# Optimization experiments

Measured on AMD Instinct MI355X. Metric: run time of the kernel, lower is better.

Reference implementation:

```python
import jax, jax.numpy as jnp
import numpy as np

D_MODEL = 1024
NUM_HEADS = 16
HEAD_DIM = D_MODEL // NUM_HEADS
B, T = 2, 2048


def setup_inputs() -> dict:
    key = jax.random.key(0)
    kx, kq, kk, kv, ko = jax.random.split(key, 5)
    s = 1.0 / np.sqrt(D_MODEL)  # ~Linear init scale
    return {
        "x": jax.random.normal(kx, (B, T, D_MODEL), dtype=jnp.float32),
        "Wq": jax.random.normal(kq, (D_MODEL, D_MODEL), dtype=jnp.float32) * s,
        "Wk": jax.random.normal(kk, (D_MODEL, D_MODEL), dtype=jnp.float32) * s,
        "Wv": jax.random.normal(kv, (D_MODEL, D_MODEL), dtype=jnp.float32) * s,
        "Wo": jax.random.normal(ko, (D_MODEL, D_MODEL), dtype=jnp.float32) * s,
    }


def reference(x, Wq, Wk, Wv, Wo):
    Bc, Tc, _ = x.shape
    H, D = NUM_HEADS, HEAD_DIM
    scale = jnp.sqrt(jnp.asarray(D, x.dtype))
    # torch Linear (bias=False): y = x @ W^T
    q = (x @ Wq.T).reshape(Bc, Tc, H, D).transpose(0, 2, 1, 3)  # [B,H,T,D]
    k = (x @ Wk.T).reshape(Bc, Tc, H, D).transpose(0, 2, 1, 3)
    v = (x @ Wv.T).reshape(Bc, Tc, H, D).transpose(0, 2, 1, 3)
    scores = jnp.einsum("bhtd,bhsd->bhts", q, k) / scale  # [B,H,T,T]
    # causal bias: upper triangle (strictly future positions) gets -1e9
    causal_bias = jnp.triu(jnp.ones((Tc, Tc), dtype=jnp.float32), k=1) * -1e9
    scores = scores + causal_bias
    weights = jax.nn.softmax(scores, axis=-1)
    # dropout is identity in eval / p=0
    out = jnp.einsum("bhts,bhsd->bhtd", weights, v)  # [B,H,T,D]
    out = out.transpose(0, 2, 1, 3).reshape(Bc, Tc, H * D)
    return out @ Wo.T
```

## Files before the change

### kernel.cpp

```cpp
#include <hip/hip_runtime.h>
#include <hip/hip_bf16.h>

typedef __bf16 bf16_t;
typedef __bf16 bf16x2 __attribute__((ext_vector_type(2)));
typedef __bf16 bf16x4 __attribute__((ext_vector_type(4)));
typedef __bf16 bf16x8 __attribute__((ext_vector_type(8)));
typedef float  f32x4  __attribute__((ext_vector_type(4)));
typedef int    i32x2  __attribute__((ext_vector_type(2)));

#define D_MODEL 1024
#define HEADS   16
#define HD      64
#define BB      2
#define TT      2048
#define MROWS   (BB*TT)

#define GLDS16(g, l) __builtin_amdgcn_global_load_lds( \
    (const __attribute__((address_space(1))) void*)(g), \
    (__attribute__((address_space(3))) void*)(l), 16, 0, 0)

static __device__ __forceinline__ int pack_bf16(float a, float b) {
    bf16x2 t; t[0] = (bf16_t)a; t[1] = (bf16_t)b;
    return __builtin_bit_cast(int, t);
}

__global__ __launch_bounds__(256) void cvt_all_kernel(const float* __restrict__ x,
                                                      const float* __restrict__ wq,
                                                      const float* __restrict__ wk,
                                                      const float* __restrict__ wv,
                                                      const float* __restrict__ wo,
                                                      bf16_t* __restrict__ dst) {
    const int i = blockIdx.x * 256 + threadIdx.x;
    const float* src;
    int s;
    if (i < 1048576) { src = x; s = i; }
    else {
        int j = i - 1048576;
        int w = j >> 18;
        s = j & 262143;
        src = (w == 0) ? wq : (w == 1) ? wk : (w == 2) ? wv : wo;
    }
    float4 v = reinterpret_cast<const float4*>(src)[s];
    bf16x4 o;
    o[0] = (bf16_t)v.x; o[1] = (bf16_t)v.y; o[2] = (bf16_t)v.z; o[3] = (bf16_t)v.w;
    reinterpret_cast<bf16x4*>(dst)[i] = o;
}

template<int MODE, int BN>
__global__ __launch_bounds__(256) void gemm_bt(const bf16_t* __restrict__ A,
                                               const bf16_t* __restrict__ Bw,
                                               void* __restrict__ Cout,
                                               int M, int N, int K) {
    constexpr int NI = BN / 32;
    __shared__ __align__(16) bf16_t As[128*32];
    __shared__ __align__(16) bf16_t Bs[BN*32];
    const int tid   = threadIdx.x;
    const int lane  = tid & 63;
    const int wave  = tid >> 6;
    const int col16 = lane & 15;
    const int quad  = lane >> 4;
    const int wrow  = (wave & 1) * 64;
    const int wcol  = (wave >> 1) * (BN / 2);
    const int bm    = blockIdx.y * 128;
    const int bn    = blockIdx.x * BN;

    const int lr = tid >> 2;
    const int lc = (tid & 3) * 8;

    const bf16_t* agp = &A [(size_t)(bm + lr)*K + lc];
    const bf16_t* bgp = &Bw[(size_t)(bn + lr)*K + lc];
    const size_t half = (size_t)64 * K;
    bf16_t* as_lo = &As[wave*512];
    bf16_t* as_hi = &As[2048 + wave*512];
    bf16_t* bs_lo = &Bs[wave*512];
    bf16_t* bs_hi = &Bs[2048 + wave*512];

    f32x4 acc[4][NI];
#pragma unroll
    for (int i = 0; i < 4; i++)
#pragma unroll
        for (int j = 0; j < NI; j++) acc[i][j] = (f32x4){0.f, 0.f, 0.f, 0.f};

    for (int k0 = 0; k0 < K; k0 += 32) {
        GLDS16(agp + k0,        as_lo);
        GLDS16(agp + half + k0, as_hi);
        GLDS16(bgp + k0,        bs_lo);
        if (BN == 128) GLDS16(bgp + half + k0, bs_hi);
        __syncthreads();

        bf16x8 af[4], bfr[NI];
#pragma unroll
        for (int mi = 0; mi < 4; mi++)
            af[mi] = *reinterpret_cast<const bf16x8*>(&As[(wrow + mi*16 + col16)*32 + quad*8]);
#pragma unroll
        for (int ni = 0; ni < NI; ni++)
            bfr[ni] = *reinterpret_cast<const bf16x8*>(&Bs[(wcol + ni*16 + col16)*32 + quad*8]);
#pragma unroll
        for (int mi = 0; mi < 4; mi++)
#pragma unroll
            for (int ni = 0; ni < NI; ni++)
                acc[mi][ni] = __builtin_amdgcn_mfma_f32_16x16x32_bf16(af[mi], bfr[ni], acc[mi][ni], 0, 0, 0);
        __syncthreads();
    }

#pragma unroll
    for (int mi = 0; mi < 4; mi++) {
#pragma unroll
        for (int r = 0; r < 4; r++) {
            const int gm = bm + wrow + mi*16 + quad*4 + r;
            const int t  = gm & (TT - 1);
            const int b  = gm >> 11;
#pragma unroll
            for (int ni = 0; ni < NI; ni++) {
                const int gn = bn + wcol + ni*16 + col16;
                float v = acc[mi][ni][r];
                if (MODE == 2) {
                    reinterpret_cast<float*>(Cout)[(size_t)gm * N + gn] = v;
                } else {
                    const int which = gn >> 10;
                    if (which == 0) v *= 0.18033688f;
                    const int n = gn & 1023;
                    const int h = n >> 6, d = n & 63;
                    const size_t off = (size_t)(which == 2 ? 3 : which) * MROWS * D_MODEL;
                    bf16_t* base = reinterpret_cast<bf16_t*>(Cout) + off;
                    base[(((size_t)(b*HEADS + h))*TT + t)*HD + d] = (bf16_t)v;
                }
            }
        }
    }
}

__global__ __launch_bounds__(256) void transpose_v(const bf16_t* __restrict__ V,
                                                   bf16_t* __restrict__ Vt) {
    __shared__ bf16_t tile[64][72];
    const int tid = threadIdx.x;
    const int bh = blockIdx.y;
    const int t0 = blockIdx.x * 64;
    const bf16_t* src = V + ((size_t)bh * TT + t0) * HD;
#pragma unroll
    for (int i = 0; i < 2; i++) {
        const int r = i*32 + (tid >> 3), c = (tid & 7) * 8;
        *reinterpret_cast<bf16x8*>(&tile[r][c]) =
            *reinterpret_cast<const bf16x8*>(&src[(size_t)r * HD + c]);
    }
    __syncthreads();
    bf16_t* dst = Vt + (size_t)bh * HD * TT + t0;
#pragma unroll
    for (int i = 0; i < 2; i++) {
        const int d = i*32 + (tid >> 3), tc = (tid & 7) * 8;
        bf16x8 o;
#pragma unroll
        for (int j = 0; j < 8; j++) o[j] = tile[tc + j][d];
        *reinterpret_cast<bf16x8*>(&dst[(size_t)d * TT + tc]) = o;
    }
}

__global__ __launch_bounds__(256, 4) void attn_kernel(const bf16_t* __restrict__ Q,
                                                      const bf16_t* __restrict__ Kk,
                                                      const bf16_t* __restrict__ Vt,
                                                      bf16_t* __restrict__ O) {
    __shared__ __align__(16) bf16_t Ks[2][64*64];
    __shared__ __align__(16) bf16_t Vs[2][64*64];

    const int tid   = threadIdx.x;
    const int lane  = tid & 63;
    const int wave  = tid >> 6;
    const int col16 = lane & 15;
    const int quad  = lane >> 4;
    const int kw    = wave & 1;
    const int qw    = wave >> 1;

    const int bx = blockIdx.x;
    const int r_ = bx >> 8, s_ = bx & 255;
    const int bh = s_ & 31;
    const int g  = s_ >> 5;
    const int qt = (r_ == 0) ? (31 - g)
                 : (r_ == 1) ? g
                 : (r_ == 2) ? (15 - g)
                             : (16 + g);
    const int qb    = qt * 64;
    const int qbase = qb + qw * 32;
    const int nkt   = qt + 1;

    const bf16_t* Qb = Q  + (size_t)bh * TT * HD;
    const bf16_t* Kb = Kk + (size_t)bh * TT * HD;
    const bf16_t* Vb = Vt + (size_t)bh * HD * TT;

    bf16x8 qf[2][2];
#pragma unroll
    for (int qg = 0; qg < 2; qg++)
#pragma unroll
        for (int h = 0; h < 2; h++)
            qf[qg][h] = *reinterpret_cast<const bf16x8*>(
                &Qb[(size_t)(qbase + qg*16 + col16)*HD + h*32 + quad*8]);

    const int srow = (tid >> 3) & 31;
    const int sg   = ((lane & 7) ^ (srow & 7)) * 8;

    auto stage = [&](int kt, int buf) {
        const int s0 = kt * 64;
        GLDS16(&Kb[(size_t)(s0 + srow)*HD + sg],        &Ks[buf][wave*512]);
        GLDS16(&Kb[(size_t)(s0 + srow + 32)*HD + sg],   &Ks[buf][2048 + wave*512]);
        GLDS16(&Vb[(size_t)srow*TT + s0 + sg],          &Vs[buf][wave*512]);
        GLDS16(&Vb[(size_t)(srow + 32)*TT + s0 + sg],   &Vs[buf][2048 + wave*512]);
    };

    f32x4 acc[4][2];
#pragma unroll
    for (int i = 0; i < 4; i++)
#pragma unroll
        for (int j = 0; j < 2; j++) acc[i][j] = (f32x4){0.f,0.f,0.f,0.f};
    float lsum[2] = {0.f, 0.f};

    const int x7 = col16 & 7;

    stage(0, 0);
    __syncthreads();

    for (int kt = 0; kt < nkt; kt++) {
        const int buf = kt & 1;
        if (kt + 1 < nkt) stage(kt + 1, buf ^ 1);
        const int s0 = kt * 64;
        const bool diag = (kt == nkt - 1);

        bf16x8 kf0[2], kf1[2];
#pragma unroll
        for (int c = 0; c < 2; c++) {
            kf0[c] = *reinterpret_cast<const bf16x8*>(
                &Ks[buf][(kw*32 + c*16 + col16)*64 + ((0*4 + quad) ^ x7)*8]);
            kf1[c] = *reinterpret_cast<const bf16x8*>(
                &Ks[buf][(kw*32 + c*16 + col16)*64 + ((1*4 + quad) ^ x7)*8]);
        }

        int pk[2][2][2];
#pragma unroll
        for (int c = 0; c < 2; c++) {
#pragma unroll
            for (int qg = 0; qg < 2; qg++) {
                __builtin_amdgcn_s_setprio(1);
                f32x4 sv = __builtin_amdgcn_mfma_f32_16x16x32_bf16(kf0[c], qf[qg][0], (f32x4){0.f,0.f,0.f,0.f}, 0, 0, 0);
                sv       = __builtin_amdgcn_mfma_f32_16x16x32_bf16(kf1[c], qf[qg][1], sv, 0, 0, 0);
                __builtin_amdgcn_s_setprio(0);

                float pr[4];
#pragma unroll
                for (int r = 0; r < 4; r++) pr[r] = exp2f(sv[r]);
                if (diag) {
#pragma unroll
                    for (int r = 0; r < 4; r++)
                        if (s0 + kw*32 + c*16 + quad*4 + r > qbase + qg*16 + col16) pr[r] = 0.f;
                }
                lsum[qg] += (pr[0] + pr[1]) + (pr[2] + pr[3]);
                pk[c][qg][0] = pack_bf16(pr[0], pr[1]);
                pk[c][qg][1] = pack_bf16(pr[2], pr[3]);
            }
        }

        bf16x8 pf[2];
#pragma unroll
        for (int qg = 0; qg < 2; qg++) {
#if __has_builtin(__builtin_amdgcn_permlane32_swap)
            i32x2 u0 = __builtin_amdgcn_permlane32_swap(pk[0][qg][0], pk[1][qg][0], false, false);
            i32x2 v0 = __builtin_amdgcn_permlane16_swap(u0[0], u0[1], false, false);
            i32x2 u1 = __builtin_amdgcn_permlane32_swap(pk[0][qg][1], pk[1][qg][1], false, false);
            i32x2 v1 = __builtin_amdgcn_permlane16_swap(u1[0], u1[1], false, false);
            int4 bi = { v0[0], v1[0], v0[1], v1[1] };
#else
            const int a1 = ((quad & 1) * 32 + col16) * 4;
            const int a2 = a1 + 64;
            const bool hi = quad >= 2;
            int b0l = __builtin_amdgcn_ds_bpermute(a1, pk[0][qg][0]);
            int b0h = __builtin_amdgcn_ds_bpermute(a1, pk[1][qg][0]);
            int b1l = __builtin_amdgcn_ds_bpermute(a1, pk[0][qg][1]);
            int b1h = __builtin_amdgcn_ds_bpermute(a1, pk[1][qg][1]);
            int b2l = __builtin_amdgcn_ds_bpermute(a2, pk[0][qg][0]);
            int b2h = __builtin_amdgcn_ds_bpermute(a2, pk[1][qg][0]);
            int b3l = __builtin_amdgcn_ds_bpermute(a2, pk[0][qg][1]);
            int b3h = __builtin_amdgcn_ds_bpermute(a2, pk[1][qg][1]);
            int4 bi = { hi ? b0h : b0l, hi ? b1h : b1l, hi ? b2h : b2l, hi ? b3h : b3l };
#endif
            pf[qg] = __builtin_bit_cast(bf16x8, bi);
        }
        __builtin_amdgcn_s_setprio(1);
#pragma unroll
        for (int c = 0; c < 4; c++) {
            bf16x8 vf = *reinterpret_cast<const bf16x8*>(
                &Vs[buf][(c*16 + col16)*64 + ((kw*4 + quad) ^ x7)*8]);
            acc[c][0] = __builtin_amdgcn_mfma_f32_16x16x32_bf16(vf, pf[0], acc[c][0], 0, 0, 0);
            acc[c][1] = __builtin_amdgcn_mfma_f32_16x16x32_bf16(vf, pf[1], acc[c][1], 0, 0, 0);
        }
        __builtin_amdgcn_s_setprio(0);
        __syncthreads();
    }

#pragma unroll
    for (int qg = 0; qg < 2; qg++) {
        lsum[qg] += __shfl_xor(lsum[qg], 16);
        lsum[qg] += __shfl_xor(lsum[qg], 32);
    }

    float* Mq = qw ? reinterpret_cast<float*>(&Vs[0][0])
                   : reinterpret_cast<float*>(&Ks[0][0]);
    float* LS = reinterpret_cast<float*>(&Vs[0][0]) + 32*68;

    if (kw == 1) {
#pragma unroll
        for (int c = 0; c < 4; c++)
#pragma unroll
            for (int qg = 0; qg < 2; qg++)
                *reinterpret_cast<f32x4*>(&Mq[(qg*16 + col16)*68 + c*16 + quad*4]) = acc[c][qg];
        if (lane < 16) {
            LS[qw*32 + lane]      = lsum[0];
            LS[qw*32 + 16 + lane] = lsum[1];
        }
    }
    __syncthreads();

    if (kw == 0) {
        const int b_ = bh >> 4, h = bh & 15;
#pragma unroll
        for (int qg = 0; qg < 2; qg++) {
            const float l   = lsum[qg] + LS[qw*32 + qg*16 + col16];
            const float inv = 1.0f / l;
            const int t = qbase + qg*16 + col16;
            bf16_t* Ob = &O[(((size_t)(b_*TT + t))*HEADS + h)*HD + quad*4];
#pragma unroll
            for (int c = 0; c < 4; c++) {
                f32x4 m = *reinterpret_cast<const f32x4*>(&Mq[(qg*16 + col16)*68 + c*16 + quad*4]);
                bf16x4 o4;
#pragma unroll
                for (int r = 0; r < 4; r++) o4[r] = (bf16_t)((acc[c][qg][r] + m[r]) * inv);
                *reinterpret_cast<bf16x4*>(&Ob[c*16]) = o4;
            }
        }
    }
}

extern "C" void kernel_launch(void* const* d_in, const int* in_sizes, int n_in,
                              void* d_out, int out_size, void* d_ws, size_t ws_size,
                              hipStream_t stream) {
    const float* x  = (const float*)d_in[0];
    const float* Wq = (const float*)d_in[1];
    const float* Wk = (const float*)d_in[2];
    const float* Wv = (const float*)d_in[3];
    const float* Wo = (const float*)d_in[4];
    float* out = (float*)d_out;

    bf16_t* Xb  = (bf16_t*)d_ws;
    bf16_t* Wqb = Xb  + (size_t)MROWS * D_MODEL;
    bf16_t* Wob = Wqb + (size_t)3 * D_MODEL * D_MODEL;
    bf16_t* Qw  = Wob + (size_t)D_MODEL * D_MODEL;
    bf16_t* Kw  = Qw  + (size_t)MROWS * D_MODEL;
    bf16_t* Vt  = Kw  + (size_t)MROWS * D_MODEL;
    bf16_t* Ow  = Vt  + (size_t)MROWS * D_MODEL;

    cvt_all_kernel<<<(MROWS*D_MODEL + 4*D_MODEL*D_MODEL) / 4 / 256, 256, 0, stream>>>(
        x, Wq, Wk, Wv, Wo, Xb);

    dim3 gqkv(3 * D_MODEL / 128, MROWS / 128);
    gemm_bt<0,128><<<gqkv, 256, 0, stream>>>(Xb, Wqb, Qw, MROWS, 3 * D_MODEL, D_MODEL);

    dim3 gt(TT / 64, BB * HEADS);
    transpose_v<<<gt, 256, 0, stream>>>(Ow, Vt);

    attn_kernel<<<dim3(1024), 256, 0, stream>>>(Qw, Kw, Vt, Ow);

    dim3 go(D_MODEL / 64, MROWS / 128);
    gemm_bt<2,64><<<go, 256, 0, stream>>>(Ow, Wob, out, MROWS, D_MODEL, D_MODEL);
}
```

Measured before the change: 183.7 us.

## Double GEMM K-tile to 64 with XOR-swizzled LDS layout

The projection GEMM now stages a 64-wide K slice per iteration instead of 32, halving the number of barrier pairs. Each 16-byte chunk is placed in LDS at a column index XORed with the row, so the wider 128-byte rows do not cause bank conflicts on fragment reads. Launch bounds now request 3 blocks per CU. The cost is doubled shared memory per block and more live fragment registers, which may limit occupancy.

Result: faster. 172.8 us (-6.0%).

```diff
diff --git a/kernel.cpp b/kernel.cpp
--- a/kernel.cpp
+++ b/kernel.cpp
@@ -47,13 +47,13 @@
 }
 
 template<int MODE, int BN>
-__global__ __launch_bounds__(256) void gemm_bt(const bf16_t* __restrict__ A,
-                                               const bf16_t* __restrict__ Bw,
-                                               void* __restrict__ Cout,
-                                               int M, int N, int K) {
+__global__ __launch_bounds__(256, 3) void gemm_bt(const bf16_t* __restrict__ A,
+                                                  const bf16_t* __restrict__ Bw,
+                                                  void* __restrict__ Cout,
+                                                  int M, int N, int K) {
     constexpr int NI = BN / 32;
-    __shared__ __align__(16) bf16_t As[128*32];
-    __shared__ __align__(16) bf16_t Bs[BN*32];
+    __shared__ __align__(16) bf16_t As[128*64];
+    __shared__ __align__(16) bf16_t Bs[BN*64];
     const int tid   = threadIdx.x;
     const int lane  = tid & 63;
     const int wave  = tid >> 6;
@@ -63,17 +63,13 @@
     const int wcol  = (wave >> 1) * (BN / 2);
     const int bm    = blockIdx.y * 128;
     const int bn    = blockIdx.x * BN;
-
-    const int lr = tid >> 2;
-    const int lc = (tid & 3) * 8;
+    const int x7    = col16 & 7;
+
+    const int lr = tid >> 3;
+    const int lc = ((tid & 7) ^ (lr & 7)) * 8;
 
     const bf16_t* agp = &A [(size_t)(bm + lr)*K + lc];
     const bf16_t* bgp = &Bw[(size_t)(bn + lr)*K + lc];
-    const size_t half = (size_t)64 * K;
-    bf16_t* as_lo = &As[wave*512];
-    bf16_t* as_hi = &As[2048 + wave*512];
-    bf16_t* bs_lo = &Bs[wave*512];
-    bf16_t* bs_hi = &Bs[2048 + wave*512];
 
     f32x4 acc[4][NI];
 #pragma unroll
@@ -81,25 +77,35 @@
 #pragma unroll
         for (int j = 0; j < NI; j++) acc[i][j] = (f32x4){0.f, 0.f, 0.f, 0.f};
 
-    for (int k0 = 0; k0 < K; k0 += 32) {
-        GLDS16(agp + k0,        as_lo);
-        GLDS16(agp + half + k0, as_hi);
-        GLDS16(bgp + k0,        bs_lo);
-        if (BN == 128) GLDS16(bgp + half + k0, bs_hi);
+    for (int k0 = 0; k0 < K; k0 += 64) {
+#pragma unroll
+        for (int s = 0; s < 4; s++)
+            GLDS16(agp + k0 + (size_t)s*32*K, &As[s*2048 + wave*512]);
+#pragma unroll
+        for (int s = 0; s < BN/32; s++)
+            GLDS16(bgp + k0 + (size_t)s*32*K, &Bs[s*2048 + wave*512]);
         __syncthreads();
 
-        bf16x8 af[4], bfr[NI];
+        bf16x8 af[4][2], bfr[NI][2];
 #pragma unroll
         for (int mi = 0; mi < 4; mi++)
-            af[mi] = *reinterpret_cast<const bf16x8*>(&As[(wrow + mi*16 + col16)*32 + quad*8]);
+#pragma unroll
+            for (int h = 0; h < 2; h++)
+                af[mi][h] = *reinterpret_cast<const bf16x8*>(
+                    &As[(wrow + mi*16 + col16)*64 + ((h*4 + quad) ^ x7)*8]);
 #pragma unroll
         for (int ni = 0; ni < NI; ni++)
-            bfr[ni] = *reinterpret_cast<const bf16x8*>(&Bs[(wcol + ni*16 + col16)*32 + quad*8]);
+#pragma unroll
+            for (int h = 0; h < 2; h++)
+                bfr[ni][h] = *reinterpret_cast<const bf16x8*>(
+                    &Bs[(wcol + ni*16 + col16)*64 + ((h*4 + quad) ^ x7)*8]);
 #pragma unroll
         for (int mi = 0; mi < 4; mi++)
 #pragma unroll
-            for (int ni = 0; ni < NI; ni++)
-                acc[mi][ni] = __builtin_amdgcn_mfma_f32_16x16x32_bf16(af[mi], bfr[ni], acc[mi][ni], 0, 0, 0);
+            for (int ni = 0; ni < NI; ni++) {
+                acc[mi][ni] = __builtin_amdgcn_mfma_f32_16x16x32_bf16(af[mi][0], bfr[ni][0], acc[mi][ni], 0, 0, 0);
+                acc[mi][ni] = __builtin_amdgcn_mfma_f32_16x16x32_bf16(af[mi][1], bfr[ni][1], acc[mi][ni], 0, 0, 0);
+            }
         __syncthreads();
     }
 
```
